# Kernel tuning notes

Hardware: AMD Instinct MI355X
Metric: run time of the kernel (lower is better)

Reference implementation:

```python
import jax, jax.numpy as jnp
import numpy as np

T, D, H, KEXP = 91, 256, 4, 4
DH = D // H
NA, NRG = 128, 1024
NEG = -1e10
SCALE = 2.0  # sqrt(head_num=4), faithful to the original (NOT sqrt(dh))


def _ln(x, g, b, eps=1e-5):
    m = jnp.mean(x, axis=-1, keepdims=True)
    v = jnp.mean((x - m) ** 2, axis=-1, keepdims=True)
    return (x - m) * jax.lax.rsqrt(v + eps) * g + b


def setup_inputs() -> dict:
    key = jax.random.key(0)
    ks = jax.random.split(key, 16)
    s = lambda fan_in: 1.0 / np.sqrt(fan_in)
    inp = {
        "agent": jax.random.normal(ks[0], (NA, T, D), jnp.float32),
        "rg": jax.random.normal(ks[1], (NRG, T, D), jnp.float32),
        "ln_x_g": jnp.ones((D,), jnp.float32),
        "ln_x_b": jnp.zeros((D,), jnp.float32),
        "wk": jax.random.uniform(ks[2], (D, D), jnp.float32, -s(D), s(D)),
        "bk": jnp.zeros((D,), jnp.float32),
        "wv": jax.random.uniform(ks[3], (D, D), jnp.float32, -s(D), s(D)),
        "bv": jnp.zeros((D,), jnp.float32),
        "wq": jax.random.uniform(ks[4], (D, D), jnp.float32, -s(D), s(D)),
        "bq": jnp.zeros((D,), jnp.float32),
        "q_scale": jnp.full((DH,), 0.001, jnp.float32),
        "wy": jax.random.uniform(ks[5], (D, D), jnp.float32, -s(D), s(D)),
        "by": jnp.zeros((D,), jnp.float32),
        "wf1": jax.random.uniform(ks[6], (D, KEXP * D), jnp.float32, -s(D), s(D)),
        "bf1": jnp.zeros((KEXP * D,), jnp.float32),
        "wf2": jax.random.uniform(ks[7], (KEXP * D, D), jnp.float32, -s(KEXP * D), s(KEXP * D)),
        "bf2": jnp.zeros((D,), jnp.float32),
        "ln_z_g": jnp.ones((D,), jnp.float32),
        "ln_z_b": jnp.zeros((D,), jnp.float32),
        "agent_rg_mask": jax.random.randint(ks[8], (T, NA, NRG), 0, 2).astype(bool),
        "padding_mask": jax.random.randint(ks[9], (T, NRG), 0, 2).astype(bool),
        "rg_valid_mask": jax.random.randint(ks[10], (T, NA), 0, 2).astype(bool),
    }
    return inp


def reference(agent, rg, ln_x_g, ln_x_b, wk, bk, wv, bv, wq, bq, q_scale,
              wy, by, wf1, bf1, wf2, bf2, ln_z_g, ln_z_b,
              agent_rg_mask, padding_mask, rg_valid_mask):
    agent_n = _ln(agent, ln_x_g, ln_x_b)   # (Na, T, D)
    rg_n = _ln(rg, ln_x_g, ln_x_b)         # (Nrg, T, D)

    K = jax.nn.relu(rg_n @ wk + bk).reshape(NRG, T, H, DH)
    V = jax.nn.relu(rg_n @ wv + bv).reshape(NRG, T, H, DH)
    Q = jax.nn.relu(agent_n @ wq + bq).reshape(NA, T, H, DH) * q_scale

    # energy: (T, H, Na, Nrg)
    energy = jnp.einsum("athd,rthd->thar", Q, K) / SCALE
    energy = jnp.where(agent_rg_mask[:, None, :, :], energy, NEG)
    energy = jnp.where(padding_mask[:, None, None, :], energy, NEG)
    energy = jnp.where(rg_valid_mask[:, None, :, None], energy, NEG)
    attn = jax.nn.softmax(energy, axis=-1)

    Y1 = jnp.einsum("thar,rthd->athd", attn, V).reshape(NA, T, D)
    Y2 = jax.nn.relu(Y1 @ wy + by)
    S = Y2 + agent_n
    F1 = jax.nn.relu(S @ wf1 + bf1)
    F2 = jax.nn.relu(F1 @ wf2 + bf2)
    Z = _ln(F2, ln_z_g, ln_z_b)

    Qp = jnp.transpose(Q, (1, 2, 0, 3))  # (T,H,Na,dh)
    Kp = jnp.transpose(K, (1, 2, 0, 3))
    Vp = jnp.transpose(V, (1, 2, 0, 3))
    return (Z, Qp, Kp, Vp)
```

## Files before the change

kernel.cpp:

```cpp
#include <hip/hip_runtime.h>

#define T_   91
#define D_   256
#define H_   4
#define DH_  64
#define NA_  128
#define NRG_ 1024
#define KEXP_ 4

typedef float f32x4 __attribute__((ext_vector_type(4)));
typedef short bf16x8 __attribute__((ext_vector_type(8)));

static constexpr float P_EPS = 1.3877787807814457e-17f;

__device__ inline ushort f2bf(float f) {
    union { float f; unsigned u; } v; v.f = f;
    unsigned r = (v.u + 0x7fffu + ((v.u >> 16) & 1u)) >> 16;
    return (ushort)r;
}
__device__ inline unsigned pk2(float a, float b) {
    return (unsigned)f2bf(a) | ((unsigned)f2bf(b) << 16);
}
__device__ inline float bf2f(ushort b) {
    union { unsigned u; float f; } v; v.u = ((unsigned)b) << 16;
    return v.f;
}

__global__ __launch_bounds__(256) void ln_norm(
    const float* __restrict__ agent, const float* __restrict__ rg,
    const float* __restrict__ g, const float* __restrict__ b,
    ushort* __restrict__ agn, ushort* __restrict__ rgn) {
    int row = blockIdx.x * 4 + (threadIdx.x >> 6);
    int lane = threadIdx.x & 63;
    bool is_a = row < NA_ * T_;
    const float* src = is_a ? (agent + (size_t)row * D_)
                            : (rg + (size_t)(row - NA_ * T_) * D_);
    f32x4 x = *(const f32x4*)(src + lane * 4);
    float s1 = x[0] + x[1] + x[2] + x[3];
    float s2 = x[0] * x[0] + x[1] * x[1] + x[2] * x[2] + x[3] * x[3];
#pragma unroll
    for (int off = 1; off < 64; off <<= 1) {
        s1 += __shfl_xor(s1, off);
        s2 += __shfl_xor(s2, off);
    }
    float mean = s1 * (1.0f / 256.0f);
    float var = s2 * (1.0f / 256.0f) - mean * mean;
    float rstd = rsqrtf(var + 1e-5f);
    f32x4 gv = *(const f32x4*)(g + lane * 4);
    f32x4 bv = *(const f32x4*)(b + lane * 4);
    float y0 = (x[0] - mean) * rstd * gv[0] + bv[0];
    float y1 = (x[1] - mean) * rstd * gv[1] + bv[1];
    float y2 = (x[2] - mean) * rstd * gv[2] + bv[2];
    float y3 = (x[3] - mean) * rstd * gv[3] + bv[3];
    ushort* dst = is_a ? (agn + (size_t)row * D_)
                       : (rgn + (size_t)(row - NA_ * T_) * D_);
    *(uint2*)(dst + lane * 4) = make_uint2(pk2(y0, y1), pk2(y2, y3));
}

__global__ __launch_bounds__(256) void prep_w_all(
    const float* __restrict__ wk, const float* __restrict__ wv,
    const float* __restrict__ wq, const float* __restrict__ wy,
    const float* __restrict__ wf1, const float* __restrict__ wf2,
    ushort* __restrict__ wkvt, ushort* __restrict__ wqt,
    ushort* __restrict__ wyt, ushort* __restrict__ wf1t,
    ushort* __restrict__ wf2t) {
    int idx = blockIdx.x * 256 + threadIdx.x;
    if (idx < 131072) {
        const float* W = (idx < 65536) ? wk : wv;
        int li = idx & 65535;
        int n = li >> 8, k = li & 255;
        wkvt[idx] = f2bf(W[(size_t)k * 256 + n]);
    } else if (idx < 196608) {
        int li = idx - 131072;
        int n = li >> 8, k = li & 255;
        wqt[li] = f2bf(wq[(size_t)k * 256 + n]);
    } else if (idx < 262144) {
        int li = idx - 196608;
        int n = li >> 8, k = li & 255;
        wyt[li] = f2bf(wy[(size_t)k * 256 + n]);
    } else if (idx < 524288) {
        int li = idx - 262144;
        int n = li >> 8, k = li & 255;
        wf1t[li] = f2bf(wf1[(size_t)k * 1024 + n]);
    } else {
        int li = idx - 524288;
        int n = li >> 10, k = li & 1023;
        wf2t[li] = f2bf(wf2[(size_t)k * 256 + n]);
    }
}

__global__ __launch_bounds__(256) void pack_mask(
    const int* __restrict__ am, const int* __restrict__ pm,
    const int* __restrict__ vmk, unsigned* __restrict__ cm) {
    int base = blockIdx.x * 4;
    int t = base / NA_;
    int w = threadIdx.x >> 6, lane = threadIdx.x & 63;
    __shared__ int pmS[NRG_];
#pragma unroll
    for (int i = 0; i < 4; ++i)
        pmS[threadIdx.x + i * 256] = pm[(size_t)t * NRG_ + threadIdx.x + i * 256];
    __syncthreads();
    int idx = base + w;
    int a = idx & (NA_ - 1);
    int valid = vmk[t * NA_ + a];
    const int* amrow = am + (size_t)idx * NRG_;
#pragma unroll
    for (int c = 0; c < 16; ++c) {
        int r = c * 64 + lane;
        bool bit = valid && amrow[r] && pmS[r];
        unsigned long long msk = __ballot(bit);
        if (lane == 0) {
            cm[(size_t)idx * 32 + c * 2]     = (unsigned)msk;
            cm[(size_t)idx * 32 + c * 2 + 1] = (unsigned)(msk >> 32);
        }
    }
}

__global__ __launch_bounds__(512) void gemm_wide(
    const ushort* __restrict__ Ab, const ushort* __restrict__ Bt,
    const float* __restrict__ bias0, const float* __restrict__ bias1,
    const float* __restrict__ aux0, const ushort* __restrict__ residb,
    float* __restrict__ out0, float* __restrict__ out1,
    ushort* __restrict__ out2, ushort* __restrict__ out3,
    int N, int K, int mode) {
    __shared__ ushort smem[64 * 72 + 256 * 72];
    __shared__ float lnp[2][64][4];
    ushort (*As)[72] = (ushort(*)[72])smem;
    ushort (*Bs)[72] = (ushort(*)[72])(smem + 64 * 72);
    float (*Et)[68] = (float(*)[68])smem;

    int bxi, by;
    if (mode == 1) {
        int wg = blockIdx.x;
        int sub = wg & 15, pid = wg >> 4;
        bxi = sub >> 3;
        by = pid * 8 + (sub & 7);
    } else {
        bxi = blockIdx.x; by = blockIdx.y;
    }
    int bn = bxi * 256;
    int bm = by * 64;
    int t = 0, rb = 0, a0 = 0;
    if (mode == 1) { t = by >> 4; rb = (by & 15) << 6; }
    else if (mode == 2) { t = by >> 1; a0 = (by & 1) << 6; }

    int tid = threadIdx.x;
    int w = tid >> 6, lane = tid & 63;
    int wm = w >> 2, wn = w & 3;
    int l15 = lane & 15, l4 = lane >> 4;

    f32x4 acc[2][4];
#pragma unroll
    for (int i = 0; i < 2; ++i)
#pragma unroll
        for (int j = 0; j < 4; ++j)
#pragma unroll
            for (int r = 0; r < 4; ++r) acc[i][j][r] = 0.0f;

    for (int k0 = 0; k0 < K; k0 += 64) {
        {
            int row = tid >> 3, c8 = (tid & 7) * 8;
            size_t arow = (mode == 1) ? ((size_t)(rb + row) * T_ + t)
                        : (mode == 2) ? ((size_t)(a0 + row) * T_ + t)
                        : (size_t)(bm + row);
            *(bf16x8*)&As[row][c8] = *(const bf16x8*)(Ab + arow * K + k0 + c8);
        }
#pragma unroll
        for (int it = 0; it < 4; ++it) {
            int li = tid + it * 512;
            int row = li >> 3, c8 = (li & 7) * 8;
            *(bf16x8*)&Bs[row][c8] =
                *(const bf16x8*)(Bt + (size_t)(bn + row) * K + k0 + c8);
        }
        __syncthreads();
#pragma unroll
        for (int kk = 0; kk < 2; ++kk) {
            bf16x8 af[2], bfr[4];
#pragma unroll
            for (int i = 0; i < 2; ++i)
                af[i] = *(const bf16x8*)&As[wm * 32 + i * 16 + l15][kk * 32 + l4 * 8];
#pragma unroll
            for (int j = 0; j < 4; ++j)
                bfr[j] = *(const bf16x8*)&Bs[wn * 64 + j * 16 + l15][kk * 32 + l4 * 8];
#pragma unroll
            for (int i = 0; i < 2; ++i)
#pragma unroll
                for (int j = 0; j < 4; ++j)
                    acc[i][j] = __builtin_amdgcn_mfma_f32_16x16x32_bf16(
                        af[i], bfr[j], acc[i][j], 0, 0, 0);
        }
        __syncthreads();
    }

    float v[2][4][4];
#pragma unroll
    for (int i = 0; i < 2; ++i)
#pragma unroll
        for (int j = 0; j < 4; ++j)
#pragma unroll
            for (int reg = 0; reg < 4; ++reg) {
                int nl = wn * 64 + j * 16 + l15;
                int rowl = wm * 32 + i * 16 + l4 * 4 + reg;
                float bs;
                if (mode == 1) bs = bxi ? bias1[nl] : bias0[nl];
                else if (mode == 0) bs = bias0[bn + nl];
                else bs = bias0[nl];
                float x = fmaxf(acc[i][j][reg] + bs, 0.0f);
                if (mode == 2) x *= aux0[nl & 63];
                if (mode == 3) x += bf2f(residb[(size_t)(bm + rowl) * 256 + nl]);
                v[i][j][reg] = x;
            }

    if (mode == 5) {
        float rs_[2][4], rq_[2][4];
#pragma unroll
        for (int i = 0; i < 2; ++i)
#pragma unroll
            for (int reg = 0; reg < 4; ++reg) {
                float s = 0.0f, q = 0.0f;
#pragma unroll
                for (int j = 0; j < 4; ++j) {
                    float x = v[i][j][reg];
                    s += x; q += x * x;
                }
#pragma unroll
                for (int off = 1; off < 16; off <<= 1) {
                    s += __shfl_xor(s, off);
                    q += __shfl_xor(q, off);
                }
                rs_[i][reg] = s; rq_[i][reg] = q;
            }
        if (l15 == 0) {
#pragma unroll
            for (int i = 0; i < 2; ++i)
#pragma unroll
                for (int reg = 0; reg < 4; ++reg) {
                    int row = wm * 32 + i * 16 + l4 * 4 + reg;
                    lnp[0][row][wn] = rs_[i][reg];
                    lnp[1][row][wn] = rq_[i][reg];
                }
        }
        __syncthreads();
#pragma unroll
        for (int i = 0; i < 2; ++i)
#pragma unroll
            for (int reg = 0; reg < 4; ++reg) {
                int row = wm * 32 + i * 16 + l4 * 4 + reg;
                float S1 = lnp[0][row][0] + lnp[0][row][1] + lnp[0][row][2] + lnp[0][row][3];
                float S2 = lnp[1][row][0] + lnp[1][row][1] + lnp[1][row][2] + lnp[1][row][3];
                float mean = S1 * (1.0f / 256.0f);
                float var = S2 * (1.0f / 256.0f) - mean * mean;
                float rstd = rsqrtf(var + 1e-5f);
#pragma unroll
                for (int j = 0; j < 4; ++j) {
                    int nl = wn * 64 + j * 16 + l15;
                    float z = (v[i][j][reg] - mean) * rstd * bias1[nl] + aux0[nl];
                    out0[(size_t)(bm + row) * 256 + nl] = z;
                }
            }
        return;
    }

#pragma unroll 1
    for (int jq = 0; jq < 4; ++jq) {
        __syncthreads();
        if (wn == jq) {
#pragma unroll
            for (int i = 0; i < 2; ++i)
#pragma unroll
                for (int j = 0; j < 4; ++j)
#pragma unroll
                    for (int reg = 0; reg < 4; ++reg)
                        Et[wm * 32 + i * 16 + l4 * 4 + reg][j * 16 + l15] = v[i][j][reg];
        }
        __syncthreads();

        if (mode == 1) {
            size_t base = (((size_t)t * H_ + jq) * NRG_ + rb) * DH_;
            float* of = bxi ? out1 : out0;
#pragma unroll
            for (int it = 0; it < 2; ++it) {
                int slot = it * 512 + tid;
                int row = slot >> 4, c4 = (slot & 15) * 4;
                *(f32x4*)(of + base + row * 64 + c4) = *(f32x4*)&Et[row][c4];
            }
            if (!bxi) {
#pragma unroll
                for (int it = 0; it < 2; ++it) {
                    int slot = it * 512 + tid;
                    int row = slot >> 4, c4 = (slot & 15) * 4;
                    uint2 u = make_uint2(pk2(Et[row][c4], Et[row][c4 + 1]),
                                         pk2(Et[row][c4 + 2], Et[row][c4 + 3]));
                    *(uint2*)(out2 + base + row * 64 + c4) = u;
                }
            } else {
                __syncthreads();
                if (wn == jq) {
#pragma unroll
                    for (int i = 0; i < 2; ++i)
#pragma unroll
                        for (int j = 0; j < 4; ++j)
#pragma unroll
                            for (int reg = 0; reg < 4; ++reg)
                                Et[j * 16 + l15][wm * 32 + i * 16 + l4 * 4 + reg] = v[i][j][reg];
                }
                __syncthreads();
                size_t tb = ((size_t)t * H_ + jq) * DH_ * NRG_;
#pragma unroll
                for (int it = 0; it < 2; ++it) {
                    int slot = it * 512 + tid;
                    int d = slot >> 4, r4 = (slot & 15) * 4;
                    uint2 u = make_uint2(pk2(Et[d][r4], Et[d][r4 + 1]),
                                         pk2(Et[d][r4 + 2], Et[d][r4 + 3]));
                    *(uint2*)(out3 + tb + (size_t)d * NRG_ + rb + r4) = u;
                }
            }
        } else if (mode == 2) {
            size_t base = (((size_t)t * H_ + jq) * NA_ + a0) * DH_;
#pragma unroll
            for (int it = 0; it < 2; ++it) {
                int slot = it * 512 + tid;
                int row = slot >> 4, c4 = (slot & 15) * 4;
                *(f32x4*)(out0 + base + row * 64 + c4) = *(f32x4*)&Et[row][c4];
                uint2 u = make_uint2(pk2(Et[row][c4] * 0.5f, Et[row][c4 + 1] * 0.5f),
                                     pk2(Et[row][c4 + 2] * 0.5f, Et[row][c4 + 3] * 0.5f));
                *(uint2*)(out2 + base + row * 64 + c4) = u;
            }
        } else {
#pragma unroll
            for (int it = 0; it < 2; ++it) {
                int slot = it * 512 + tid;
                int row = slot >> 4, c4 = (slot & 15) * 4;
                uint2 u = make_uint2(pk2(Et[row][c4], Et[row][c4 + 1]),
                                     pk2(Et[row][c4 + 2], Et[row][c4 + 3]));
                *(uint2*)(out2 + (size_t)(bm + row) * N + bn + jq * 64 + c4) = u;
            }
        }
    }
}

__global__ __launch_bounds__(512) void attn_flash(
    const ushort* __restrict__ Qb, const ushort* __restrict__ Kb,
    const ushort* __restrict__ Vtb, const unsigned* __restrict__ cm,
    ushort* __restrict__ Y1b) {
    int th = blockIdx.x;
    int t = th >> 2, h = th & 3;
    int tid = threadIdx.x;
    int w = tid >> 6, lane = tid & 63;
    int l15 = lane & 15, l4 = lane >> 4;

    __shared__ ushort Ks[64][72];
    __shared__ ushort Vts[64][72];
    __shared__ ushort Ps[128][72];
    __shared__ unsigned cmw[128][2];

    bf16x8 qf[2];
#pragma unroll
    for (int kk = 0; kk < 2; ++kk)
        qf[kk] = *(const bf16x8*)(Qb + ((size_t)th * NA_ + w * 16 + l15) * DH_
                                  + kk * 32 + l4 * 8);

    f32x4 o[4];
    float rsum[4] = {0.0f, 0.0f, 0.0f, 0.0f};
#pragma unroll
    for (int ds = 0; ds < 4; ++ds)
#pragma unroll
        for (int r = 0; r < 4; ++r) o[ds][r] = 0.0f;

    for (int rt = 0; rt < 16; ++rt) {
        int r0 = rt * 64;
        {
            int row = tid >> 3, c8 = (tid & 7) * 8;
            *(bf16x8*)&Ks[row][c8] =
                *(const bf16x8*)(Kb + ((size_t)th * NRG_ + r0 + row) * DH_ + c8);
            *(bf16x8*)&Vts[row][c8] =
                *(const bf16x8*)(Vtb + ((size_t)th * DH_ + row) * NRG_ + r0 + c8);
        }
        if (tid < 256) {
            int a = tid >> 1, wd = tid & 1;
            cmw[a][wd] = cm[((size_t)t * NA_ + a) * 32 + rt * 2 + wd];
        }
        __syncthreads();

        f32x4 e[4];
#pragma unroll
        for (int rs = 0; rs < 4; ++rs) {
#pragma unroll
            for (int r = 0; r < 4; ++r) e[rs][r] = 0.0f;
#pragma unroll
            for (int kk = 0; kk < 2; ++kk) {
                bf16x8 kf = *(const bf16x8*)&Ks[rs * 16 + l15][kk * 32 + l4 * 8];
                e[rs] = __builtin_amdgcn_mfma_f32_16x16x32_bf16(qf[kk], kf, e[rs], 0, 0, 0);
            }
        }

#pragma unroll
        for (int reg = 0; reg < 4; ++reg) {
            int a_loc = w * 16 + l4 * 4 + reg;
            unsigned w0 = cmw[a_loc][0], w1 = cmw[a_loc][1];
#pragma unroll
            for (int rs = 0; rs < 4; ++rs) {
                unsigned wd = (rs & 2) ? w1 : w0;
                int bit = (wd >> ((rs & 1) * 16 + l15)) & 1;
                float p = bit ? __expf(e[rs][reg]) : P_EPS;
                rsum[reg] += p;
                Ps[a_loc][rs * 16 + l15] = f2bf(p);
            }
        }

#pragma unroll
        for (int rc = 0; rc < 2; ++rc) {
            bf16x8 pa = *(const bf16x8*)&Ps[w * 16 + l15][rc * 32 + l4 * 8];
#pragma unroll
            for (int ds = 0; ds < 4; ++ds) {
                bf16x8 vf = *(const bf16x8*)&Vts[ds * 16 + l15][rc * 32 + l4 * 8];
                o[ds] = __builtin_amdgcn_mfma_f32_16x16x32_bf16(pa, vf, o[ds], 0, 0, 0);
            }
        }
        __syncthreads();
    }

#pragma unroll
    for (int off = 1; off < 16; off <<= 1)
#pragma unroll
        for (int reg = 0; reg < 4; ++reg)
            rsum[reg] += __shfl_xor(rsum[reg], off);
    float rinv[4];
#pragma unroll
    for (int reg = 0; reg < 4; ++reg) rinv[reg] = 1.0f / rsum[reg];

#pragma unroll
    for (int ds = 0; ds < 4; ++ds)
#pragma unroll
        for (int reg = 0; reg < 4; ++reg) {
            int a_g = w * 16 + l4 * 4 + reg;
            int d = ds * 16 + l15;
            Y1b[((size_t)a_g * T_ + t) * D_ + h * DH_ + d] = f2bf(o[ds][reg] * rinv[reg]);
        }
}

extern "C" void kernel_launch(void* const* d_in, const int* in_sizes, int n_in,
                              void* d_out, int out_size, void* d_ws, size_t ws_size,
                              hipStream_t stream) {
    const float* agent   = (const float*)d_in[0];
    const float* rg      = (const float*)d_in[1];
    const float* ln_x_g  = (const float*)d_in[2];
    const float* ln_x_b  = (const float*)d_in[3];
    const float* wk      = (const float*)d_in[4];
    const float* bk      = (const float*)d_in[5];
    const float* wv      = (const float*)d_in[6];
    const float* bv      = (const float*)d_in[7];
    const float* wq      = (const float*)d_in[8];
    const float* bq      = (const float*)d_in[9];
    const float* q_scale = (const float*)d_in[10];
    const float* wy      = (const float*)d_in[11];
    const float* by      = (const float*)d_in[12];
    const float* wf1     = (const float*)d_in[13];
    const float* bf1     = (const float*)d_in[14];
    const float* wf2     = (const float*)d_in[15];
    const float* bf2     = (const float*)d_in[16];
    const float* ln_z_g  = (const float*)d_in[17];
    const float* ln_z_b  = (const float*)d_in[18];
    const int*   am      = (const int*)d_in[19];
    const int*   pm      = (const int*)d_in[20];
    const int*   vmk     = (const int*)d_in[21];

    float* Z  = (float*)d_out;
    float* Qp = Z + (size_t)NA_ * T_ * D_;
    float* Kp = Qp + (size_t)NA_ * T_ * D_;
    float* Vp = Kp + (size_t)NRG_ * T_ * D_;

    char* p = (char*)d_ws;
    ushort* rgn_b = (ushort*)p;   p += (size_t)NRG_ * T_ * D_ * 2;
    ushort* agn_b = (ushort*)p;   p += (size_t)NA_ * T_ * D_ * 2;
    ushort* wkvt  = (ushort*)p;   p += (size_t)512 * 256 * 2;
    ushort* wqt   = (ushort*)p;   p += (size_t)256 * 256 * 2;
    ushort* wyt   = (ushort*)p;   p += (size_t)256 * 256 * 2;
    ushort* wf1t  = (ushort*)p;   p += (size_t)1024 * 256 * 2;
    ushort* wf2t  = (ushort*)p;   p += (size_t)256 * 1024 * 2;
    unsigned* cm  = (unsigned*)p; p += (size_t)T_ * NA_ * 32 * 4;
    ushort* Kb    = (ushort*)p;   p += (size_t)T_ * H_ * NRG_ * DH_ * 2;
    ushort* Vtb   = (ushort*)p;   p += (size_t)T_ * H_ * NRG_ * DH_ * 2;
    ushort* Qb    = (ushort*)p;   p += (size_t)T_ * H_ * NA_ * DH_ * 2;
    ushort* Y1b   = (ushort*)p;   p += (size_t)NA_ * T_ * D_ * 2;
    ushort* Sb    = (ushort*)p;   p += (size_t)NA_ * T_ * D_ * 2;

    ushort* F1b = rgn_b;

    dim3 blk(256), wblk(512);

    ln_norm<<<dim3((NA_ + NRG_) * T_ / 4), blk, 0, stream>>>(
        agent, rg, ln_x_g, ln_x_b, agn_b, rgn_b);

    prep_w_all<<<dim3(3072), blk, 0, stream>>>(
        wk, wv, wq, wy, wf1, wf2, wkvt, wqt, wyt, wf1t, wf2t);

    pack_mask<<<dim3(T_ * NA_ / 4), blk, 0, stream>>>(am, pm, vmk, cm);

    gemm_wide<<<dim3(T_ * 32), wblk, 0, stream>>>(
        rgn_b, wkvt, bk, bv, nullptr, nullptr,
        Kp, Vp, Kb, Vtb, 512, 256, 1);

    gemm_wide<<<dim3(1, T_ * 2), wblk, 0, stream>>>(
        agn_b, wqt, bq, nullptr, q_scale, nullptr,
        Qp, nullptr, Qb, nullptr, 256, 256, 2);

    attn_flash<<<dim3(T_ * H_), wblk, 0, stream>>>(Qb, Kb, Vtb, cm, Y1b);

    gemm_wide<<<dim3(1, NA_ * T_ / 64), wblk, 0, stream>>>(
        Y1b, wyt, by, nullptr, nullptr, agn_b,
        nullptr, nullptr, Sb, nullptr, 256, 256, 3);

    gemm_wide<<<dim3(4, NA_ * T_ / 64), wblk, 0, stream>>>(
        Sb, wf1t, bf1, nullptr, nullptr, nullptr,
        nullptr, nullptr, F1b, nullptr, 1024, 256, 0);

    gemm_wide<<<dim3(1, NA_ * T_ / 64), wblk, 0, stream>>>(
        F1b, wf2t, bf2, ln_z_g, ln_z_b, nullptr,
        Z, nullptr, nullptr, nullptr, 256, 1024, 5);
}
```

Before: 292.0 us.

## Merge prep kernels, fuse KVQ GEMMs, double-buffer attention, fuse MLP chain

```diff
diff --git a/kernel.cpp b/kernel.cpp
--- a/kernel.cpp
+++ b/kernel.cpp
@@ -26,123 +26,129 @@
     return v.f;
 }
 
-__global__ __launch_bounds__(256) void ln_norm(
+#define LN_BLOCKS 26208
+#define PM_BLOCKS 2912
+#define PW_BLOCKS 3072
+
+__global__ __launch_bounds__(256) void prep_all(
     const float* __restrict__ agent, const float* __restrict__ rg,
     const float* __restrict__ g, const float* __restrict__ b,
-    ushort* __restrict__ agn, ushort* __restrict__ rgn) {
-    int row = blockIdx.x * 4 + (threadIdx.x >> 6);
-    int lane = threadIdx.x & 63;
-    bool is_a = row < NA_ * T_;
-    const float* src = is_a ? (agent + (size_t)row * D_)
-                            : (rg + (size_t)(row - NA_ * T_) * D_);
-    f32x4 x = *(const f32x4*)(src + lane * 4);
-    float s1 = x[0] + x[1] + x[2] + x[3];
-    float s2 = x[0] * x[0] + x[1] * x[1] + x[2] * x[2] + x[3] * x[3];
-#pragma unroll
-    for (int off = 1; off < 64; off <<= 1) {
-        s1 += __shfl_xor(s1, off);
-        s2 += __shfl_xor(s2, off);
-    }
-    float mean = s1 * (1.0f / 256.0f);
-    float var = s2 * (1.0f / 256.0f) - mean * mean;
-    float rstd = rsqrtf(var + 1e-5f);
-    f32x4 gv = *(const f32x4*)(g + lane * 4);
-    f32x4 bv = *(const f32x4*)(b + lane * 4);
-    float y0 = (x[0] - mean) * rstd * gv[0] + bv[0];
-    float y1 = (x[1] - mean) * rstd * gv[1] + bv[1];
-    float y2 = (x[2] - mean) * rstd * gv[2] + bv[2];
-    float y3 = (x[3] - mean) * rstd * gv[3] + bv[3];
-    ushort* dst = is_a ? (agn + (size_t)row * D_)
-                       : (rgn + (size_t)(row - NA_ * T_) * D_);
-    *(uint2*)(dst + lane * 4) = make_uint2(pk2(y0, y1), pk2(y2, y3));
-}
-
-__global__ __launch_bounds__(256) void prep_w_all(
+    const int* __restrict__ am, const int* __restrict__ pm,
+    const int* __restrict__ vmk,
     const float* __restrict__ wk, const float* __restrict__ wv,
     const float* __restrict__ wq, const float* __restrict__ wy,
     const float* __restrict__ wf1, const float* __restrict__ wf2,
+    ushort* __restrict__ agn, ushort* __restrict__ rgn,
+    unsigned* __restrict__ cm,
     ushort* __restrict__ wkvt, ushort* __restrict__ wqt,
     ushort* __restrict__ wyt, ushort* __restrict__ wf1t,
     ushort* __restrict__ wf2t) {
-    int idx = blockIdx.x * 256 + threadIdx.x;
-    if (idx < 131072) {
-        const float* W = (idx < 65536) ? wk : wv;
-        int li = idx & 65535;
-        int n = li >> 8, k = li & 255;
-        wkvt[idx] = f2bf(W[(size_t)k * 256 + n]);
-    } else if (idx < 196608) {
-        int li = idx - 131072;
-        int n = li >> 8, k = li & 255;
-        wqt[li] = f2bf(wq[(size_t)k * 256 + n]);
-    } else if (idx < 262144) {
-        int li = idx - 196608;
-        int n = li >> 8, k = li & 255;
-        wyt[li] = f2bf(wy[(size_t)k * 256 + n]);
-    } else if (idx < 524288) {
-        int li = idx - 262144;
-        int n = li >> 8, k = li & 255;
-        wf1t[li] = f2bf(wf1[(size_t)k * 1024 + n]);
+    __shared__ int pmS[NRG_];
+    int bid = blockIdx.x;
+    if (bid < LN_BLOCKS) {
+        int row = bid * 4 + (threadIdx.x >> 6);
+        int lane = threadIdx.x & 63;
+        bool is_a = row < NA_ * T_;
+        const float* src = is_a ? (agent + (size_t)row * D_)
+                                : (rg + (size_t)(row - NA_ * T_) * D_);
+        f32x4 x = *(const f32x4*)(src + lane * 4);
+        float s1 = x[0] + x[1] + x[2] + x[3];
+        float s2 = x[0] * x[0] + x[1] * x[1] + x[2] * x[2] + x[3] * x[3];
+#pragma unroll
+        for (int off = 1; off < 64; off <<= 1) {
+            s1 += __shfl_xor(s1, off);
+            s2 += __shfl_xor(s2, off);
+        }
+        float mean = s1 * (1.0f / 256.0f);
+        float var = s2 * (1.0f / 256.0f) - mean * mean;
+        float rstd = rsqrtf(var + 1e-5f);
+        f32x4 gv = *(const f32x4*)(g + lane * 4);
+        f32x4 bv = *(const f32x4*)(b + lane * 4);
+        float y0 = (x[0] - mean) * rstd * gv[0] + bv[0];
+        float y1 = (x[1] - mean) * rstd * gv[1] + bv[1];
+        float y2 = (x[2] - mean) * rstd * gv[2] + bv[2];
+        float y3 = (x[3] - mean) * rstd * gv[3] + bv[3];
+        ushort* dst = is_a ? (agn + (size_t)row * D_)
+                           : (rgn + (size_t)(row - NA_ * T_) * D_);
+        *(uint2*)(dst + lane * 4) = make_uint2(pk2(y0, y1), pk2(y2, y3));
+    } else if (bid < LN_BLOCKS + PM_BLOCKS) {
+        int base = (bid - LN_BLOCKS) * 4;
+        int t = base / NA_;
+        int w = threadIdx.x >> 6, lane = threadIdx.x & 63;
+#pragma unroll
+        for (int i = 0; i < 4; ++i)
+            pmS[threadIdx.x + i * 256] = pm[(size_t)t * NRG_ + threadIdx.x + i * 256];
+        __syncthreads();
+        int idx = base + w;
+        int a = idx & (NA_ - 1);
+        int valid = vmk[t * NA_ + a];
+        const int* amrow = am + (size_t)idx * NRG_;
+#pragma unroll
+        for (int c = 0; c < 16; ++c) {
+            int r = c * 64 + lane;
+            bool bit = valid && amrow[r] && pmS[r];
+            unsigned long long msk = __ballot(bit);
+            if (lane == 0) {
+                cm[(size_t)idx * 32 + c * 2]     = (unsigned)msk;
+                cm[(size_t)idx * 32 + c * 2 + 1] = (unsigned)(msk >> 32);
+            }
+        }
     } else {
-        int li = idx - 524288;
-        int n = li >> 10, k = li & 1023;
-        wf2t[li] = f2bf(wf2[(size_t)k * 256 + n]);
-    }
-}
-
-__global__ __launch_bounds__(256) void pack_mask(
-    const int* __restrict__ am, const int* __restrict__ pm,
-    const int* __restrict__ vmk, unsigned* __restrict__ cm) {
-    int base = blockIdx.x * 4;
-    int t = base / NA_;
-    int w = threadIdx.x >> 6, lane = threadIdx.x & 63;
-    __shared__ int pmS[NRG_];
-#pragma unroll
-    for (int i = 0; i < 4; ++i)
-        pmS[threadIdx.x + i * 256] = pm[(size_t)t * NRG_ + threadIdx.x + i * 256];
-    __syncthreads();
-    int idx = base + w;
-    int a = idx & (NA_ - 1);
-    int valid = vmk[t * NA_ + a];
-    const int* amrow = am + (size_t)idx * NRG_;
-#pragma unroll
-    for (int c = 0; c < 16; ++c) {
-        int r = c * 64 + lane;
-        bool bit = valid && amrow[r] && pmS[r];
-        unsigned long long msk = __ballot(bit);
-        if (lane == 0) {
-            cm[(size_t)idx * 32 + c * 2]     = (unsigned)msk;
-            cm[(size_t)idx * 32 + c * 2 + 1] = (unsigned)(msk >> 32);
-        }
-    }
-}
-
-__global__ __launch_bounds__(512) void gemm_wide(
-    const ushort* __restrict__ Ab, const ushort* __restrict__ Bt,
-    const float* __restrict__ bias0, const float* __restrict__ bias1,
-    const float* __restrict__ aux0, const ushort* __restrict__ residb,
-    float* __restrict__ out0, float* __restrict__ out1,
-    ushort* __restrict__ out2, ushort* __restrict__ out3,
-    int N, int K, int mode) {
+        int idx = (bid - LN_BLOCKS - PM_BLOCKS) * 256 + threadIdx.x;
+        if (idx < 131072) {
+            const float* W = (idx < 65536) ? wk : wv;
+            int li = idx & 65535;
+            int n = li >> 8, k = li & 255;
+            wkvt[idx] = f2bf(W[(size_t)k * 256 + n]);
+        } else if (idx < 196608) {
+            int li = idx - 131072;
+            int n = li >> 8, k = li & 255;
+            wqt[li] = f2bf(wq[(size_t)k * 256 + n]);
+        } else if (idx < 262144) {
+            int li = idx - 196608;
+            int n = li >> 8, k = li & 255;
+            wyt[li] = f2bf(wy[(size_t)k * 256 + n]);
+        } else if (idx < 524288) {
+            int li = idx - 262144;
+            int n = li >> 8, k = li & 255;
+            wf1t[li] = f2bf(wf1[(size_t)k * 1024 + n]);
+        } else {
+            int li = idx - 524288;
+            int n = li >> 10, k = li & 1023;
+            wf2t[li] = f2bf(wf2[(size_t)k * 256 + n]);
+        }
+    }
+}
+
+__global__ __launch_bounds__(512) void gemm_kvq(
+    const ushort* __restrict__ rgn, const ushort* __restrict__ agn,
+    const ushort* __restrict__ wkvt, const ushort* __restrict__ wqt,
+    const float* __restrict__ bk, const float* __restrict__ bv,
+    const float* __restrict__ bq, const float* __restrict__ qs,
+    float* __restrict__ Kp, float* __restrict__ Vp, float* __restrict__ Qp,
+    ushort* __restrict__ Kb, ushort* __restrict__ Vtb, ushort* __restrict__ Qb) {
     __shared__ ushort smem[64 * 72 + 256 * 72];
-    __shared__ float lnp[2][64][4];
     ushort (*As)[72] = (ushort(*)[72])smem;
     ushort (*Bs)[72] = (ushort(*)[72])(smem + 64 * 72);
     float (*Et)[68] = (float(*)[68])smem;
 
-    int bxi, by;
-    if (mode == 1) {
-        int wg = blockIdx.x;
-        int sub = wg & 15, pid = wg >> 4;
+    int bid = blockIdx.x;
+    bool isQ = bid >= 2912;
+    int bxi = 0, t, rb = 0, a0 = 0, bn = 0;
+    const ushort* Ab;
+    const ushort* Bt;
+    if (!isQ) {
+        int sub = bid & 15, pid = bid >> 4;
         bxi = sub >> 3;
-        by = pid * 8 + (sub & 7);
+        int by = pid * 8 + (sub & 7);
+        t = by >> 4; rb = (by & 15) << 6;
+        bn = bxi << 8;
+        Ab = rgn; Bt = wkvt;
     } else {
-        bxi = blockIdx.x; by = blockIdx.y;
-    }
-    int bn = bxi * 256;
-    int bm = by * 64;
-    int t = 0, rb = 0, a0 = 0;
-    if (mode == 1) { t = by >> 4; rb = (by & 15) << 6; }
-    else if (mode == 2) { t = by >> 1; a0 = (by & 1) << 6; }
+        int qid = bid - 2912;
+        t = qid >> 1; a0 = (qid & 1) << 6;
+        Ab = agn; Bt = wqt;
+    }
 
     int tid = threadIdx.x;
     int w = tid >> 6, lane = tid & 63;
@@ -157,20 +163,19 @@
 #pragma unroll
             for (int r = 0; r < 4; ++r) acc[i][j][r] = 0.0f;
 
-    for (int k0 = 0; k0 < K; k0 += 64) {
+    for (int k0 = 0; k0 < 256; k0 += 64) {
         {
             int row = tid >> 3, c8 = (tid & 7) * 8;
-            size_t arow = (mode == 1) ? ((size_t)(rb + row) * T_ + t)
-                        : (mode == 2) ? ((size_t)(a0 + row) * T_ + t)
-                        : (size_t)(bm + row);
-            *(bf16x8*)&As[row][c8] = *(const bf16x8*)(Ab + arow * K + k0 + c8);
+            size_t arow = isQ ? ((size_t)(a0 + row) * T_ + t)
+                              : ((size_t)(rb + row) * T_ + t);
+            *(bf16x8*)&As[row][c8] = *(const bf16x8*)(Ab + arow * 256 + k0 + c8);
         }
 #pragma unroll
         for (int it = 0; it < 4; ++it) {
             int li = tid + it * 512;
             int row = li >> 3, c8 = (li & 7) * 8;
             *(bf16x8*)&Bs[row][c8] =
-                *(const bf16x8*)(Bt + (size_t)(bn + row) * K + k0 + c8);
+                *(const bf16x8*)(Bt + (size_t)(bn + row) * 256 + k0 + c8);
         }
         __syncthreads();
 #pragma unroll
@@ -200,66 +205,11 @@
 #pragma unroll
             for (int reg = 0; reg < 4; ++reg) {
                 int nl = wn * 64 + j * 16 + l15;
-                int rowl = wm * 32 + i * 16 + l4 * 4 + reg;
-                float bs;
-                if (mode == 1) bs = bxi ? bias1[nl] : bias0[nl];
-                else if (mode == 0) bs = bias0[bn + nl];
-                else bs = bias0[nl];
+                float bs = isQ ? bq[nl] : (bxi ? bv[nl] : bk[nl]);
                 float x = fmaxf(acc[i][j][reg] + bs, 0.0f);
-                if (mode == 2) x *= aux0[nl & 63];
-                if (mode == 3) x += bf2f(residb[(size_t)(bm + rowl) * 256 + nl]);
+                if (isQ) x *= qs[nl & 63];
                 v[i][j][reg] = x;
             }
-
-    if (mode == 5) {
-        float rs_[2][4], rq_[2][4];
-#pragma unroll
-        for (int i = 0; i < 2; ++i)
-#pragma unroll
-            for (int reg = 0; reg < 4; ++reg) {
-                float s = 0.0f, q = 0.0f;
-#pragma unroll
-                for (int j = 0; j < 4; ++j) {
-                    float x = v[i][j][reg];
-                    s += x; q += x * x;
-                }
-#pragma unroll
-                for (int off = 1; off < 16; off <<= 1) {
-                    s += __shfl_xor(s, off);
-                    q += __shfl_xor(q, off);
-                }
-                rs_[i][reg] = s; rq_[i][reg] = q;
-            }
-        if (l15 == 0) {
-#pragma unroll
-            for (int i = 0; i < 2; ++i)
-#pragma unroll
-                for (int reg = 0; reg < 4; ++reg) {
-                    int row = wm * 32 + i * 16 + l4 * 4 + reg;
-                    lnp[0][row][wn] = rs_[i][reg];
-                    lnp[1][row][wn] = rq_[i][reg];
-                }
-        }
-        __syncthreads();
-#pragma unroll
-        for (int i = 0; i < 2; ++i)
-#pragma unroll
-            for (int reg = 0; reg < 4; ++reg) {
-                int row = wm * 32 + i * 16 + l4 * 4 + reg;
-                float S1 = lnp[0][row][0] + lnp[0][row][1] + lnp[0][row][2] + lnp[0][row][3];
-                float S2 = lnp[1][row][0] + lnp[1][row][1] + lnp[1][row][2] + lnp[1][row][3];
-                float mean = S1 * (1.0f / 256.0f);
-                float var = S2 * (1.0f / 256.0f) - mean * mean;
-                float rstd = rsqrtf(var + 1e-5f);
-#pragma unroll
-                for (int j = 0; j < 4; ++j) {
-                    int nl = wn * 64 + j * 16 + l15;
-                    float z = (v[i][j][reg] - mean) * rstd * bias1[nl] + aux0[nl];
-                    out0[(size_t)(bm + row) * 256 + nl] = z;
-                }
-            }
-        return;
-    }
 
 #pragma unroll 1
     for (int jq = 0; jq < 4; ++jq) {
@@ -275,9 +225,20 @@
         }
         __syncthreads();
 
-        if (mode == 1) {
+        if (isQ) {
+            size_t base = (((size_t)t * H_ + jq) * NA_ + a0) * DH_;
+#pragma unroll
+            for (int it = 0; it < 2; ++it) {
+                int slot = it * 512 + tid;
+                int row = slot >> 4, c4 = (slot & 15) * 4;
+                *(f32x4*)(Qp + base + row * 64 + c4) = *(f32x4*)&Et[row][c4];
+                uint2 u = make_uint2(pk2(Et[row][c4] * 0.5f, Et[row][c4 + 1] * 0.5f),
+                                     pk2(Et[row][c4 + 2] * 0.5f, Et[row][c4 + 3] * 0.5f));
+                *(uint2*)(Qb + base + row * 64 + c4) = u;
+            }
+        } else {
             size_t base = (((size_t)t * H_ + jq) * NRG_ + rb) * DH_;
-            float* of = bxi ? out1 : out0;
+            float* of = bxi ? Vp : Kp;
 #pragma unroll
             for (int it = 0; it < 2; ++it) {
                 int slot = it * 512 + tid;
@@ -291,7 +252,7 @@
                     int row = slot >> 4, c4 = (slot & 15) * 4;
                     uint2 u = make_uint2(pk2(Et[row][c4], Et[row][c4 + 1]),
                                          pk2(Et[row][c4 + 2], Et[row][c4 + 3]));
-                    *(uint2*)(out2 + base + row * 64 + c4) = u;
+                    *(uint2*)(Kb + base + row * 64 + c4) = u;
                 }
             } else {
                 __syncthreads();
@@ -312,28 +273,8 @@
                     int d = slot >> 4, r4 = (slot & 15) * 4;
                     uint2 u = make_uint2(pk2(Et[d][r4], Et[d][r4 + 1]),
                                          pk2(Et[d][r4 + 2], Et[d][r4 + 3]));
-                    *(uint2*)(out3 + tb + (size_t)d * NRG_ + rb + r4) = u;
+                    *(uint2*)(Vtb + tb + (size_t)d * NRG_ + rb + r4) = u;
                 }
-            }
-        } else if (mode == 2) {
-            size_t base = (((size_t)t * H_ + jq) * NA_ + a0) * DH_;
-#pragma unroll
-            for (int it = 0; it < 2; ++it) {
-                int slot = it * 512 + tid;
-                int row = slot >> 4, c4 = (slot & 15) * 4;
-                *(f32x4*)(out0 + base + row * 64 + c4) = *(f32x4*)&Et[row][c4];
-                uint2 u = make_uint2(pk2(Et[row][c4] * 0.5f, Et[row][c4 + 1] * 0.5f),
-                                     pk2(Et[row][c4 + 2] * 0.5f, Et[row][c4 + 3] * 0.5f));
-                *(uint2*)(out2 + base + row * 64 + c4) = u;
-            }
-        } else {
-#pragma unroll
-            for (int it = 0; it < 2; ++it) {
-                int slot = it * 512 + tid;
-                int row = slot >> 4, c4 = (slot & 15) * 4;
-                uint2 u = make_uint2(pk2(Et[row][c4], Et[row][c4 + 1]),
-                                     pk2(Et[row][c4 + 2], Et[row][c4 + 3]));
-                *(uint2*)(out2 + (size_t)(bm + row) * N + bn + jq * 64 + c4) = u;
             }
         }
     }
@@ -349,10 +290,10 @@
     int w = tid >> 6, lane = tid & 63;
     int l15 = lane & 15, l4 = lane >> 4;
 
-    __shared__ ushort Ks[64][72];
-    __shared__ ushort Vts[64][72];
+    __shared__ ushort Ks[2][64][72];
+    __shared__ ushort Vts[2][64][72];
     __shared__ ushort Ps[128][72];
-    __shared__ unsigned cmw[128][2];
+    __shared__ unsigned cmAll[128][33];
 
     bf16x8 qf[2];
 #pragma unroll
@@ -360,6 +301,25 @@
         qf[kk] = *(const bf16x8*)(Qb + ((size_t)th * NA_ + w * 16 + l15) * DH_
                                   + kk * 32 + l4 * 8);
 
+    {
+        const uint4* src = (const uint4*)(cm + (size_t)t * NA_ * 32 + tid * 8);
+        uint4 c0 = src[0], c1 = src[1];
+        int a = tid >> 2, wd = (tid & 3) * 8;
+        cmAll[a][wd + 0] = c0.x; cmAll[a][wd + 1] = c0.y;
+        cmAll[a][wd + 2] = c0.z; cmAll[a][wd + 3] = c0.w;
+        cmAll[a][wd + 4] = c1.x; cmAll[a][wd + 5] = c1.y;
+        cmAll[a][wd + 6] = c1.z; cmAll[a][wd + 7] = c1.w;
+    }
+
+    int srow = tid >> 3, sc8 = (tid & 7) * 8;
+    const ushort* Kbase = Kb + (size_t)th * NRG_ * DH_;
+    const ushort* Vbase = Vtb + (size_t)th * DH_ * NRG_;
+    bf16x8 kreg = *(const bf16x8*)(Kbase + (size_t)srow * DH_ + sc8);
+    bf16x8 vreg = *(const bf16x8*)(Vbase + (size_t)srow * NRG_ + sc8);
+    *(bf16x8*)&Ks[0][srow][sc8] = kreg;
+    *(bf16x8*)&Vts[0][srow][sc8] = vreg;
+    __syncthreads();
+
     f32x4 o[4];
     float rsum[4] = {0.0f, 0.0f, 0.0f, 0.0f};
 #pragma unroll
@@ -368,19 +328,12 @@
         for (int r = 0; r < 4; ++r) o[ds][r] = 0.0f;
 
     for (int rt = 0; rt < 16; ++rt) {
-        int r0 = rt * 64;
-        {
-            int row = tid >> 3, c8 = (tid & 7) * 8;
-            *(bf16x8*)&Ks[row][c8] =
-                *(const bf16x8*)(Kb + ((size_t)th * NRG_ + r0 + row) * DH_ + c8);
-            *(bf16x8*)&Vts[row][c8] =
-                *(const bf16x8*)(Vtb + ((size_t)th * DH_ + row) * NRG_ + r0 + c8);
-        }
-        if (tid < 256) {
-            int a = tid >> 1, wd = tid & 1;
-            cmw[a][wd] = cm[((size_t)t * NA_ + a) * 32 + rt * 2 + wd];
-        }
-        __syncthreads();
+        int cur = rt & 1;
+        if (rt < 15) {
+            int r0n = (rt + 1) * 64;
+            kreg = *(const bf16x8*)(Kbase + (size_t)(r0n + srow) * DH_ + sc8);
+            vreg = *(const bf16x8*)(Vbase + (size_t)srow * NRG_ + r0n + sc8);
+        }
 
         f32x4 e[4];
 #pragma unroll
@@ -389,7 +342,7 @@
             for (int r = 0; r < 4; ++r) e[rs][r] = 0.0f;
 #pragma unroll
             for (int kk = 0; kk < 2; ++kk) {
-                bf16x8 kf = *(const bf16x8*)&Ks[rs * 16 + l15][kk * 32 + l4 * 8];
+                bf16x8 kf = *(const bf16x8*)&Ks[cur][rs * 16 + l15][kk * 32 + l4 * 8];
                 e[rs] = __builtin_amdgcn_mfma_f32_16x16x32_bf16(qf[kk], kf, e[rs], 0, 0, 0);
             }
         }
@@ -397,7 +350,7 @@
 #pragma unroll
         for (int reg = 0; reg < 4; ++reg) {
             int a_loc = w * 16 + l4 * 4 + reg;
-            unsigned w0 = cmw[a_loc][0], w1 = cmw[a_loc][1];
+            unsigned w0 = cmAll[a_loc][rt * 2], w1 = cmAll[a_loc][rt * 2 + 1];
 #pragma unroll
             for (int rs = 0; rs < 4; ++rs) {
                 unsigned wd = (rs & 2) ? w1 : w0;
@@ -413,11 +366,16 @@
             bf16x8 pa = *(const bf16x8*)&Ps[w * 16 + l15][rc * 32 + l4 * 8];
 #pragma unroll
             for (int ds = 0; ds < 4; ++ds) {
-                bf16x8 vf = *(const bf16x8*)&Vts[ds * 16 + l15][rc * 32 + l4 * 8];
+                bf16x8 vf = *(const bf16x8*)&Vts[cur][ds * 16 + l15][rc * 32 + l4 * 8];
                 o[ds] = __builtin_amdgcn_mfma_f32_16x16x32_bf16(pa, vf, o[ds], 0, 0, 0);
             }
         }
-        __syncthreads();
+
+        if (rt < 15) {
+            *(bf16x8*)&Ks[cur ^ 1][srow][sc8] = kreg;
+            *(bf16x8*)&Vts[cur ^ 1][srow][sc8] = vreg;
+            __syncthreads();
+        }
     }
 
 #pragma unroll
@@ -437,6 +395,147 @@
             int d = ds * 16 + l15;
             Y1b[((size_t)a_g * T_ + t) * D_ + h * DH_ + d] = f2bf(o[ds][reg] * rinv[reg]);
         }
+}
+
+__global__ __launch_bounds__(512) void mlp_fused(
+    const ushort* __restrict__ Y1b, const ushort* __restrict__ agn,
+    const ushort* __restrict__ wyt, const ushort* __restrict__ wf1t,
+    const ushort* __restrict__ wf2t,
+    const float* __restrict__ by, const float* __restrict__ bf1,
+    const float* __restrict__ bf2,
+    const float* __restrict__ lng, const float* __restrict__ lnb,
+    float* __restrict__ Z) {
+    __shared__ ushort Ss[16][264];
+    __shared__ ushort F1s[16][1032];
+    __shared__ float lnp[2][16][8];
+    ushort (*Y1s)[264] = (ushort(*)[264])&F1s[0][0];
+    float (*Zs)[260] = (float(*)[260])&F1s[0][0];
+
+    int m0 = blockIdx.x * 16;
+    int tid = threadIdx.x;
+    int w = tid >> 6, lane = tid & 63;
+    int l15 = lane & 15, l4 = lane >> 4;
+
+    {
+        int row = tid >> 5, c8 = (tid & 31) * 8;
+        *(bf16x8*)&Y1s[row][c8] = *(const bf16x8*)(Y1b + (size_t)(m0 + row) * 256 + c8);
+    }
+    __syncthreads();
+    f32x4 acc1[2];
+#pragma unroll
+    for (int j = 0; j < 2; ++j)
+#pragma unroll
+        for (int r = 0; r < 4; ++r) acc1[j][r] = 0.0f;
+#pragma unroll
+    for (int kk = 0; kk < 8; ++kk) {
+        bf16x8 af = *(const bf16x8*)&Y1s[l15][kk * 32 + l4 * 8];
+#pragma unroll
+        for (int j = 0; j < 2; ++j) {
+            bf16x8 bfr = *(const bf16x8*)(wyt + (size_t)(w * 32 + j * 16 + l15) * 256
+                                          + kk * 32 + l4 * 8);
+            acc1[j] = __builtin_amdgcn_mfma_f32_16x16x32_bf16(af, bfr, acc1[j], 0, 0, 0);
+        }
+    }
+    __syncthreads();
+#pragma unroll
+    for (int j = 0; j < 2; ++j)
+#pragma unroll
+        for (int reg = 0; reg < 4; ++reg) {
+            int row = l4 * 4 + reg;
+            int n = w * 32 + j * 16 + l15;
+            float x = fmaxf(acc1[j][reg] + by[n], 0.0f)
+                    + bf2f(agn[(size_t)(m0 + row) * 256 + n]);
+            Ss[row][n] = f2bf(x);
+        }
+    __syncthreads();
+
+    f32x4 acc2[8];
+#pragma unroll
+    for (int j = 0; j < 8; ++j)
+#pragma unroll
+        for (int r = 0; r < 4; ++r) acc2[j][r] = 0.0f;
+#pragma unroll
+    for (int kk = 0; kk < 8; ++kk) {
+        bf16x8 af = *(const bf16x8*)&Ss[l15][kk * 32 + l4 * 8];
+#pragma unroll
+        for (int j = 0; j < 8; ++j) {
+            bf16x8 bfr = *(const bf16x8*)(wf1t + (size_t)(w * 128 + j * 16 + l15) * 256
+                                          + kk * 32 + l4 * 8);
+            acc2[j] = __builtin_amdgcn_mfma_f32_16x16x32_bf16(af, bfr, acc2[j], 0, 0, 0);
+        }
+    }
+#pragma unroll
+    for (int j = 0; j < 8; ++j)
+#pragma unroll
+        for (int reg = 0; reg < 4; ++reg) {
+            int row = l4 * 4 + reg;
+            int n = w * 128 + j * 16 + l15;
+            F1s[row][n] = f2bf(fmaxf(acc2[j][reg] + bf1[n], 0.0f));
+        }
+    __syncthreads();
+
+    f32x4 acc3[2];
+#pragma unroll
+    for (int j = 0; j < 2; ++j)
+#pragma unroll
+        for (int r = 0; r < 4; ++r) acc3[j][r] = 0.0f;
+#pragma unroll
+    for (int kk = 0; kk < 32; ++kk) {
+        bf16x8 af = *(const bf16x8*)&F1s[l15][kk * 32 + l4 * 8];
+#pragma unroll
+        for (int j = 0; j < 2; ++j) {
+            bf16x8 bfr = *(const bf16x8*)(wf2t + (size_t)(w * 32 + j * 16 + l15) * 1024
+                                          + kk * 32 + l4 * 8);
+            acc3[j] = __builtin_amdgcn_mfma_f32_16x16x32_bf16(af, bfr, acc3[j], 0, 0, 0);
+        }
+    }
+    float xv[2][4];
+#pragma unroll
+    for (int j = 0; j < 2; ++j)
+#pragma unroll
+        for (int reg = 0; reg < 4; ++reg) {
+            int n = w * 32 + j * 16 + l15;
+            xv[j][reg] = fmaxf(acc3[j][reg] + bf2[n], 0.0f);
+        }
+#pragma unroll
+    for (int reg = 0; reg < 4; ++reg) {
+        float s = xv[0][reg] + xv[1][reg];
+        float q = xv[0][reg] * xv[0][reg] + xv[1][reg] * xv[1][reg];
+#pragma unroll
+        for (int off = 1; off < 16; off <<= 1) {
+            s += __shfl_xor(s, off);
+            q += __shfl_xor(q, off);
+        }
+        if (l15 == 0) {
+            int row = l4 * 4 + reg;
+            lnp[0][row][w] = s;
+            lnp[1][row][w] = q;
+        }
+    }
+    __syncthreads();
+#pragma unroll
+    for (int reg = 0; reg < 4; ++reg) {
+        int row = l4 * 4 + reg;
+        float S1 = 0.0f, S2 = 0.0f;
+#pragma unroll
+        for (int wv = 0; wv < 8; ++wv) { S1 += lnp[0][row][wv]; S2 += lnp[1][row][wv]; }
+        float mean = S1 * (1.0f / 256.0f);
+        float var = S2 * (1.0f / 256.0f) - mean * mean;
+        float rstd = rsqrtf(var + 1e-5f);
+#pragma unroll
+        for (int j = 0; j < 2; ++j) {
+            int n = w * 32 + j * 16 + l15;
+            Zs[row][n] = (xv[j][reg] - mean) * rstd * lng[n] + lnb[n];
+        }
+    }
+    __syncthreads();
+    {
+        int row = tid >> 5, c8 = (tid & 31) * 8;
+        f32x4 z0 = *(f32x4*)&Zs[row][c8];
+        f32x4 z1 = *(f32x4*)&Zs[row][c8 + 4];
+        *(f32x4*)(Z + (size_t)(m0 + row) * 256 + c8) = z0;
+        *(f32x4*)(Z + (size_t)(m0 + row) * 256 + c8 + 4) = z1;
+    }
 }
 
 extern "C" void kernel_launch(void* const* d_in, const int* in_sizes, int n_in,
@@ -483,39 +582,18 @@
     ushort* Vtb   = (ushort*)p;   p += (size_t)T_ * H_ * NRG_ * DH_ * 2;
     ushort* Qb    = (ushort*)p;   p += (size_t)T_ * H_ * NA_ * DH_ * 2;
     ushort* Y1b   = (ushort*)p;   p += (size_t)NA_ * T_ * D_ * 2;
-    ushort* Sb    = (ushort*)p;   p += (size_t)NA_ * T_ * D_ * 2;
-
-    ushort* F1b = rgn_b;
-
-    dim3 blk(256), wblk(512);
-
-    ln_norm<<<dim3((NA_ + NRG_) * T_ / 4), blk, 0, stream>>>(
-        agent, rg, ln_x_g, ln_x_b, agn_b, rgn_b);
-
-    prep_w_all<<<dim3(3072), blk, 0, stream>>>(
-        wk, wv, wq, wy, wf1, wf2, wkvt, wqt, wyt, wf1t, wf2t);
-
-    pack_mask<<<dim3(T_ * NA_ / 4), blk, 0, stream>>>(am, pm, vmk, cm);
-
-    gemm_wide<<<dim3(T_ * 32), wblk, 0, stream>>>(
-        rgn_b, wkvt, bk, bv, nullptr, nullptr,
-        Kp, Vp, Kb, Vtb, 512, 256, 1);
-
-    gemm_wide<<<dim3(1, T_ * 2), wblk, 0, stream>>>(
-        agn_b, wqt, bq, nullptr, q_scale, nullptr,
-        Qp, nullptr, Qb, nullptr, 256, 256, 2);
-
-    attn_flash<<<dim3(T_ * H_), wblk, 0, stream>>>(Qb, Kb, Vtb, cm, Y1b);
-
-    gemm_wide<<<dim3(1, NA_ * T_ / 64), wblk, 0, stream>>>(
-        Y1b, wyt, by, nullptr, nullptr, agn_b,
-        nullptr, nullptr, Sb, nullptr, 256, 256, 3);
-
-    gemm_wide<<<dim3(4, NA_ * T_ / 64), wblk, 0, stream>>>(
-        Sb, wf1t, bf1, nullptr, nullptr, nullptr,
-        nullptr, nullptr, F1b, nullptr, 1024, 256, 0);
-
-    gemm_wide<<<dim3(1, NA_ * T_ / 64), wblk, 0, stream>>>(
-        F1b, wf2t, bf2, ln_z_g, ln_z_b, nullptr,
-        Z, nullptr, nullptr, nullptr, 256, 1024, 5);
-}
+
+    prep_all<<<dim3(LN_BLOCKS + PM_BLOCKS + PW_BLOCKS), dim3(256), 0, stream>>>(
+        agent, rg, ln_x_g, ln_x_b, am, pm, vmk,
+        wk, wv, wq, wy, wf1, wf2,
+        agn_b, rgn_b, cm, wkvt, wqt, wyt, wf1t, wf2t);
+
+    gemm_kvq<<<dim3(2912 + T_ * 2), dim3(512), 0, stream>>>(
+        rgn_b, agn_b, wkvt, wqt, bk, bv, bq, q_scale,
+        Kp, Vp, Qp, Kb, Vtb, Qb);
+
+    attn_flash<<<dim3(T_ * H_), dim3(512), 0, stream>>>(Qb, Kb, Vtb, cm, Y1b);
+
+    mlp_fused<<<dim3(NA_ * T_ / 16), dim3(512), 0, stream>>>(
+        Y1b, agn_b, wyt, wf1t, wf2t, by, bf1, bf2, ln_z_g, ln_z_b, Z);
+}
```

New measurement: 302.6 us. +3.6%, slower.
